# Kernel optimization log

Hardware: AMD Instinct MI355X
Metric: run time of the kernel (lower is better)

The kernel has to match this reference:

```python
import jax, jax.numpy as jnp
import numpy as np

B, N, F, T, KCHEB, O = 8, 1024, 64, 12, 3, 64

def setup_inputs() -> dict:
    key = jax.random.key(0)
    k1, k2, k3, k4 = jax.random.split(key, 4)
    graph_signal = jax.random.normal(k1, (B, N, F, T), dtype=jnp.float32)
    spatial_attention = jax.random.uniform(k2, (B, N, N), dtype=jnp.float32)
    # Chebyshev polynomials of scaled Laplacian, scaled to keep magnitudes sane
    cheb = jax.random.normal(k3, (KCHEB, N, N), dtype=jnp.float32) / np.float32(np.sqrt(N))
    # theta: (K, F, num_of_filters), glorot-ish scale
    theta = jax.random.normal(k4, (KCHEB, F, O), dtype=jnp.float32) / np.float32(np.sqrt(F))
    return {"graph_signal": graph_signal, "spatial_attention": spatial_attention,
            "cheb": cheb, "theta": theta}

def reference(graph_signal, spatial_attention, cheb, theta):
    # Original loops over t and k computing:
    #   rhs[b,n,f] = sum_m (T_k[m,n] * att[b,m,n]) * x[b,m,f,t]   (transposed batch_dot)
    #   out[b,n,o,t] += rhs @ theta[k]
    # Vectorized over k, t in one pass.
    Ak = cheb[:, None, :, :] * spatial_attention[None]          # (K,B,N,N) = T_k * attention
    rhs = jnp.einsum('kbmn,bmft->kbnft', Ak, graph_signal)      # T_k_with_at^T @ x for all t
    out = jnp.einsum('kbnft,kfo->bnot', rhs, theta)             # sum over k and f
    return jax.nn.relu(out)                                     # (B, N, O, T)
```

## Files before the change

kernel.cpp:

```cpp
#include <hip/hip_runtime.h>
#include <stdint.h>

#define NB 8
#define NN 1024
#define NF 64
#define NT 12
#define NK 3
#define NO 64
#define NQ 768
#define KKC 3072

typedef __attribute__((ext_vector_type(8))) short bf16x8;
typedef __attribute__((ext_vector_type(4))) float f32x4;

typedef const unsigned int __attribute__((address_space(1)))* gas1_t;
typedef unsigned int __attribute__((address_space(3)))* las3_t;

__device__ __forceinline__ void gload_lds16(const void* g, void* l) {
  __builtin_amdgcn_global_load_lds((gas1_t)g, (las3_t)l, 16, 0, 0);
}

__device__ __forceinline__ unsigned short f2bf(float f) {
  union { float f; unsigned int u; } v; v.f = f;
  unsigned int u = v.u;
  unsigned int r = (u + 0x7FFFu + ((u >> 16) & 1u)) >> 16;
  return (unsigned short)r;
}

__global__ void k0_thetaT(const float* __restrict__ theta, unsigned short* __restrict__ thT) {
  int i = blockIdx.x * 256 + threadIdx.x;
  if (i >= NK * NO * NF) return;
  int f = i & 63, o = (i >> 6) & 63, k = i >> 12;
  thT[i] = f2bf(theta[(k * NF + f) * NO + o]);
}

__global__ __launch_bounds__(256) void k123(const float* __restrict__ x,
                                            const unsigned short* __restrict__ thT,
                                            unsigned short* __restrict__ Y,
                                            const float* __restrict__ cheb,
                                            const float* __restrict__ att,
                                            unsigned short* __restrict__ A2) {
  __shared__ alignas(16) char smem[66560];
  const int bid = blockIdx.x;
  const int tid = threadIdx.x;

  if (bid < 512) {
    unsigned short* Xs = (unsigned short*)smem;
    unsigned short* Ts = (unsigned short*)(smem + 24576);
    const int mc = bid & 63;
    const int b  = bid >> 6;
    const int w = tid >> 6, l = tid & 63;
    const int lrow = l & 15, lk = l >> 4;

    const float* xb = x + ((size_t)(b * NN + mc * 16)) * (NF * NT);
#pragma unroll
    for (int u0 = 0; u0 < 2; ++u0) {
      const int u  = u0 * 256 + tid;
      const int m  = u >> 5;
      const int fp = u & 31;
      const float* src = xb + ((size_t)m * NF + fp * 2) * NT;
      float v[24];
#pragma unroll
      for (int i = 0; i < 6; ++i)
        *(float4*)(v + i * 4) = *(const float4*)(src + i * 4);
#pragma unroll
      for (int t = 0; t < 12; ++t) {
        unsigned int pk = (unsigned int)f2bf(v[t]) | ((unsigned int)f2bf(v[t + 12]) << 16);
        const int byte = (t * 2048 + m * 128 + fp * 4) ^ ((m & 7) << 4);
        *(unsigned int*)((char*)Xs + byte) = pk;
      }
    }
#pragma unroll
    for (int u0 = 0; u0 < 6; ++u0) {
      const int u  = u0 * 256 + tid;
      const int k  = u >> 9;
      const int o  = (u >> 3) & 63;
      const int f8 = u & 7;
      bf16x8 val = *(const bf16x8*)(thT + (size_t)u * 8);
      const int byte = (k * 8192 + o * 128 + f8 * 16) ^ ((o & 7) << 4);
      *(bf16x8*)((char*)Ts + byte) = val;
    }
    __syncthreads();

#pragma unroll
    for (int ti = 0; ti < 3; ++ti) {
      const int t = w * 3 + ti;
      bf16x8 af[2];
#pragma unroll
      for (int kss = 0; kss < 2; ++kss) {
        const int byte = (t * 2048 + lrow * 128 + kss * 64 + lk * 16) ^ ((lrow & 7) << 4);
        af[kss] = *(const bf16x8*)((const char*)Xs + byte);
      }
      for (int k = 0; k < NK; ++k) {
        f32x4 acc[4] = {};
#pragma unroll
        for (int kss = 0; kss < 2; ++kss) {
#pragma unroll
          for (int oj = 0; oj < 4; ++oj) {
            const int row = oj * 16 + lrow;
            const int byte = (k * 8192 + row * 128 + kss * 64 + lk * 16) ^ ((row & 7) << 4);
            bf16x8 bb = *(const bf16x8*)((const char*)Ts + byte);
            acc[oj] = __builtin_amdgcn_mfma_f32_16x16x32_bf16(af[kss], bb, acc[oj], 0, 0, 0);
          }
        }
#pragma unroll
        for (int oj = 0; oj < 4; ++oj) {
          const int o  = oj * 16 + lrow;
          const int mg = mc * 16 + lk * 4;
          uint2 u;
          u.x = (unsigned int)f2bf(acc[oj][0]) | ((unsigned int)f2bf(acc[oj][1]) << 16);
          u.y = (unsigned int)f2bf(acc[oj][2]) | ((unsigned int)f2bf(acc[oj][3]) << 16);
          size_t el = ((size_t)(b * NQ + o * NT + t)) * KKC + k * NN + mg;
          *(uint2*)(void*)(Y + el) = u;
        }
      }
    }
  } else {
    float (*att_s)[65]      = (float(*)[65])smem;
    float (*cheb_s)[64][65] = (float(*)[64][65])(smem + 16640);
    const int bid2 = bid - 512;
    const int n0 = (bid2 >> 4) * 64;
    const int m0 = (bid2 & 15) * 64;
    const int r4 = tid >> 4;
    const int c  = tid & 15;

#pragma unroll
    for (int k = 0; k < NK; ++k)
#pragma unroll
      for (int p = 0; p < 4; ++p) {
        int r = r4 + p * 16;
        const float4 v = *(const float4*)(cheb + ((size_t)(k * NN + m0 + r)) * NN + n0 + c * 4);
        cheb_s[k][r][c * 4 + 0] = v.x; cheb_s[k][r][c * 4 + 1] = v.y;
        cheb_s[k][r][c * 4 + 2] = v.z; cheb_s[k][r][c * 4 + 3] = v.w;
      }

    for (int b = 0; b < NB; ++b) {
      __syncthreads();
#pragma unroll
      for (int p = 0; p < 4; ++p) {
        int r = r4 + p * 16;
        const float4 v = *(const float4*)(att + ((size_t)(b * NN + m0 + r)) * NN + n0 + c * 4);
        att_s[r][c * 4 + 0] = v.x; att_s[r][c * 4 + 1] = v.y;
        att_s[r][c * 4 + 2] = v.z; att_s[r][c * 4 + 3] = v.w;
      }
      __syncthreads();
      for (int k = 0; k < NK; ++k) {
#pragma unroll
        for (int p = 0; p < 8; ++p) {
          int e  = p * 256 + tid;
          int jn = e >> 5;
          int q  = e & 31;
          float f0 = att_s[2 * q][jn]     * cheb_s[k][2 * q][jn];
          float f1 = att_s[2 * q + 1][jn] * cheb_s[k][2 * q + 1][jn];
          unsigned int pk = (unsigned int)f2bf(f0) | ((unsigned int)f2bf(f1) << 16);
          size_t el = ((size_t)(b * NN + n0 + jn)) * KKC + k * NN + m0 + 2 * q;
          *(unsigned int*)(A2 + el) = pk;
        }
      }
    }
  }
}

__global__ __launch_bounds__(256) void k4_main(const unsigned short* __restrict__ A2,
                                               const unsigned short* __restrict__ Y,
                                               float* __restrict__ out) {
  __shared__ unsigned short Asl[64 * 64];
  __shared__ unsigned short Bsl[128 * 64];
  const int tid = threadIdx.x;
  const int w = tid >> 6, l = tid & 63;
  const int lrow = l & 15, lk = l >> 4;
  const int wm = w >> 1, wq = w & 1;

  const int lin = (blockIdx.x & 7) * 96 + (blockIdx.x >> 3);
  const int b   = lin / 96;
  const int rem = lin % 96;
  const int bn  = rem / 6;
  const int bq  = rem % 6;

  const unsigned short* Abase = A2 + ((size_t)(b * NN + bn * 64)) * KKC;
  const unsigned short* Bbase = Y  + ((size_t)(b * NQ + bq * 128)) * KKC;

  f32x4 acc[2][4] = {};

  for (int kt = 0; kt < KKC / 64; ++kt) {
    const int kb = kt * 64;
#pragma unroll
    for (int it = 0; it < 2; ++it) {
      const int idx = it * 256 + tid;
      const int r   = idx >> 3;
      const int c16 = (idx & 7) ^ (r & 7);
      gload_lds16(Abase + (size_t)r * KKC + kb + c16 * 8, Asl + (size_t)idx * 8);
    }
#pragma unroll
    for (int it = 0; it < 4; ++it) {
      const int idx = it * 256 + tid;
      const int r   = idx >> 3;
      const int c16 = (idx & 7) ^ (r & 7);
      gload_lds16(Bbase + (size_t)r * KKC + kb + c16 * 8, Bsl + (size_t)idx * 8);
    }
    __syncthreads();
#pragma unroll
    for (int kss = 0; kss < 2; ++kss) {
      bf16x8 af[2], bfr[4];
#pragma unroll
      for (int mi = 0; mi < 2; ++mi) {
        const int row = wm * 32 + mi * 16 + lrow;
        const int sw = (row * 128 + kss * 64 + lk * 16) ^ ((row & 7) << 4);
        af[mi] = *(const bf16x8*)((const char*)Asl + sw);
      }
#pragma unroll
      for (int nj = 0; nj < 4; ++nj) {
        const int row = wq * 64 + nj * 16 + lrow;
        const int sw = (row * 128 + kss * 64 + lk * 16) ^ ((row & 7) << 4);
        bfr[nj] = *(const bf16x8*)((const char*)Bsl + sw);
      }
#pragma unroll
      for (int mi = 0; mi < 2; ++mi)
#pragma unroll
        for (int nj = 0; nj < 4; ++nj)
          acc[mi][nj] = __builtin_amdgcn_mfma_f32_16x16x32_bf16(af[mi], bfr[nj], acc[mi][nj], 0, 0, 0);
    }
    __syncthreads();
  }

  const int nb0 = bn * 64 + wm * 32;
  const int qb0 = bq * 128 + wq * 64;
#pragma unroll
  for (int mi = 0; mi < 2; ++mi) {
#pragma unroll
    for (int nj = 0; nj < 4; ++nj) {
      const int q = qb0 + nj * 16 + lrow;
#pragma unroll
      for (int j = 0; j < 4; ++j) {
        const int n = nb0 + mi * 16 + lk * 4 + j;
        float v = acc[mi][nj][j];
        out[((size_t)(b * NN + n)) * NQ + q] = v > 0.f ? v : 0.f;
      }
    }
  }
}

extern "C" void kernel_launch(void* const* d_in, const int* in_sizes, int n_in,
                              void* d_out, int out_size, void* d_ws, size_t ws_size,
                              hipStream_t stream) {
  const float* x     = (const float*)d_in[0];
  const float* att   = (const float*)d_in[1];
  const float* cheb  = (const float*)d_in[2];
  const float* theta = (const float*)d_in[3];
  float* out = (float*)d_out;

  char* ws = (char*)d_ws;
  unsigned short* A2  = (unsigned short*)(ws);
  unsigned short* Y   = (unsigned short*)(ws + 50331648);
  unsigned short* thT = (unsigned short*)(ws + 88080384);

  k0_thetaT<<<48, 256, 0, stream>>>(theta, thT);
  k123<<<768, 256, 0, stream>>>(x, thT, Y, cheb, att, A2);
  k4_main<<<768, 256, 0, stream>>>(A2, Y, out);
}
```

Baseline: 94.63 us.

## Split attention-cheb blocks per batch and load theta fragments directly into registers

The A2-producing branch now launches one block per (batch, m-tile, n-tile) instead of looping over all batches, which raises the grid from 768 to 2560 blocks and lets cheb be staged one k at a time. Shared memory drops from about 65KB to about 33KB, so more blocks can be resident per CU. The Y branch stops staging theta in LDS and loads the B fragments from global memory straight into registers once per k, reusing them across three time steps. The cost is that cheb tiles are re-read for each batch (8x more cheb traffic) and theta fragments are read from global/L2 by every block.

```diff
diff --git a/kernel.cpp b/kernel.cpp
--- a/kernel.cpp
+++ b/kernel.cpp
@@ -40,13 +40,12 @@
                                             const float* __restrict__ cheb,
                                             const float* __restrict__ att,
                                             unsigned short* __restrict__ A2) {
-  __shared__ alignas(16) char smem[66560];
+  __shared__ alignas(16) char smem[33280];
   const int bid = blockIdx.x;
   const int tid = threadIdx.x;
 
   if (bid < 512) {
     unsigned short* Xs = (unsigned short*)smem;
-    unsigned short* Ts = (unsigned short*)(smem + 24576);
     const int mc = bid & 63;
     const int b  = bid >> 6;
     const int w = tid >> 6, l = tid & 63;
@@ -70,39 +69,35 @@
         *(unsigned int*)((char*)Xs + byte) = pk;
       }
     }
-#pragma unroll
-    for (int u0 = 0; u0 < 6; ++u0) {
-      const int u  = u0 * 256 + tid;
-      const int k  = u >> 9;
-      const int o  = (u >> 3) & 63;
-      const int f8 = u & 7;
-      bf16x8 val = *(const bf16x8*)(thT + (size_t)u * 8);
-      const int byte = (k * 8192 + o * 128 + f8 * 16) ^ ((o & 7) << 4);
-      *(bf16x8*)((char*)Ts + byte) = val;
-    }
     __syncthreads();
 
+    bf16x8 af[3][2];
 #pragma unroll
     for (int ti = 0; ti < 3; ++ti) {
       const int t = w * 3 + ti;
-      bf16x8 af[2];
 #pragma unroll
       for (int kss = 0; kss < 2; ++kss) {
         const int byte = (t * 2048 + lrow * 128 + kss * 64 + lk * 16) ^ ((lrow & 7) << 4);
-        af[kss] = *(const bf16x8*)((const char*)Xs + byte);
-      }
-      for (int k = 0; k < NK; ++k) {
+        af[ti][kss] = *(const bf16x8*)((const char*)Xs + byte);
+      }
+    }
+
+    for (int k = 0; k < NK; ++k) {
+      bf16x8 bb[2][4];
+#pragma unroll
+      for (int kss = 0; kss < 2; ++kss)
+#pragma unroll
+        for (int oj = 0; oj < 4; ++oj)
+          bb[kss][oj] = *(const bf16x8*)(thT + (size_t)(k * NO + oj * 16 + lrow) * NF + kss * 32 + lk * 8);
+#pragma unroll
+      for (int ti = 0; ti < 3; ++ti) {
+        const int t = w * 3 + ti;
         f32x4 acc[4] = {};
 #pragma unroll
-        for (int kss = 0; kss < 2; ++kss) {
-#pragma unroll
-          for (int oj = 0; oj < 4; ++oj) {
-            const int row = oj * 16 + lrow;
-            const int byte = (k * 8192 + row * 128 + kss * 64 + lk * 16) ^ ((row & 7) << 4);
-            bf16x8 bb = *(const bf16x8*)((const char*)Ts + byte);
-            acc[oj] = __builtin_amdgcn_mfma_f32_16x16x32_bf16(af[kss], bb, acc[oj], 0, 0, 0);
-          }
-        }
+        for (int kss = 0; kss < 2; ++kss)
+#pragma unroll
+          for (int oj = 0; oj < 4; ++oj)
+            acc[oj] = __builtin_amdgcn_mfma_f32_16x16x32_bf16(af[ti][kss], bb[kss][oj], acc[oj], 0, 0, 0);
 #pragma unroll
         for (int oj = 0; oj < 4; ++oj) {
           const int o  = oj * 16 + lrow;
@@ -116,46 +111,42 @@
       }
     }
   } else {
-    float (*att_s)[65]      = (float(*)[65])smem;
-    float (*cheb_s)[64][65] = (float(*)[64][65])(smem + 16640);
+    float (*att_s)[65]  = (float(*)[65])smem;
+    float (*cheb_s)[65] = (float(*)[65])(smem + 16640);
     const int bid2 = bid - 512;
-    const int n0 = (bid2 >> 4) * 64;
-    const int m0 = (bid2 & 15) * 64;
+    const int n0 = (bid2 & 15) * 64;
+    const int m0 = ((bid2 >> 4) & 15) * 64;
+    const int b  = bid2 >> 8;
     const int r4 = tid >> 4;
     const int c  = tid & 15;
 
 #pragma unroll
-    for (int k = 0; k < NK; ++k)
+    for (int p = 0; p < 4; ++p) {
+      int r = r4 + p * 16;
+      const float4 v = *(const float4*)(att + ((size_t)(b * NN + m0 + r)) * NN + n0 + c * 4);
+      att_s[r][c * 4 + 0] = v.x; att_s[r][c * 4 + 1] = v.y;
+      att_s[r][c * 4 + 2] = v.z; att_s[r][c * 4 + 3] = v.w;
+    }
+    for (int k = 0; k < NK; ++k) {
+      if (k) __syncthreads();
 #pragma unroll
       for (int p = 0; p < 4; ++p) {
         int r = r4 + p * 16;
         const float4 v = *(const float4*)(cheb + ((size_t)(k * NN + m0 + r)) * NN + n0 + c * 4);
-        cheb_s[k][r][c * 4 + 0] = v.x; cheb_s[k][r][c * 4 + 1] = v.y;
-        cheb_s[k][r][c * 4 + 2] = v.z; cheb_s[k][r][c * 4 + 3] = v.w;
-      }
-
-    for (int b = 0; b < NB; ++b) {
+        cheb_s[r][c * 4 + 0] = v.x; cheb_s[r][c * 4 + 1] = v.y;
+        cheb_s[r][c * 4 + 2] = v.z; cheb_s[r][c * 4 + 3] = v.w;
+      }
       __syncthreads();
 #pragma unroll
-      for (int p = 0; p < 4; ++p) {
-        int r = r4 + p * 16;
-        const float4 v = *(const float4*)(att + ((size_t)(b * NN + m0 + r)) * NN + n0 + c * 4);
-        att_s[r][c * 4 + 0] = v.x; att_s[r][c * 4 + 1] = v.y;
-        att_s[r][c * 4 + 2] = v.z; att_s[r][c * 4 + 3] = v.w;
-      }
-      __syncthreads();
-      for (int k = 0; k < NK; ++k) {
-#pragma unroll
-        for (int p = 0; p < 8; ++p) {
-          int e  = p * 256 + tid;
-          int jn = e >> 5;
-          int q  = e & 31;
-          float f0 = att_s[2 * q][jn]     * cheb_s[k][2 * q][jn];
-          float f1 = att_s[2 * q + 1][jn] * cheb_s[k][2 * q + 1][jn];
-          unsigned int pk = (unsigned int)f2bf(f0) | ((unsigned int)f2bf(f1) << 16);
-          size_t el = ((size_t)(b * NN + n0 + jn)) * KKC + k * NN + m0 + 2 * q;
-          *(unsigned int*)(A2 + el) = pk;
-        }
+      for (int p = 0; p < 8; ++p) {
+        int e  = p * 256 + tid;
+        int jn = e >> 5;
+        int q  = e & 31;
+        float f0 = att_s[2 * q][jn]     * cheb_s[2 * q][jn];
+        float f1 = att_s[2 * q + 1][jn] * cheb_s[2 * q + 1][jn];
+        unsigned int pk = (unsigned int)f2bf(f0) | ((unsigned int)f2bf(f1) << 16);
+        size_t el = ((size_t)(b * NN + n0 + jn)) * KKC + k * NN + m0 + 2 * q;
+        *(unsigned int*)(A2 + el) = pk;
       }
     }
   }
@@ -255,6 +246,6 @@
   unsigned short* thT = (unsigned short*)(ws + 88080384);
 
   k0_thetaT<<<48, 256, 0, stream>>>(theta, thT);
-  k123<<<768, 256, 0, stream>>>(x, thT, Y, cheb, att, A2);
+  k123<<<2560, 256, 0, stream>>>(x, thT, Y, cheb, att, A2);
   k4_main<<<768, 256, 0, stream>>>(A2, Y, out);
 }
```

Measured after the change: 94.05 us. No clear change (-0.6%).
